# Performance work log

Measured on AMD Instinct MI355X. Metric: run time of the kernel, lower is better.

The kernel has to match this reference:

```python
import jax, jax.numpy as jnp
import numpy as np

B, S, HID = 1, 2048, 2048
H, KV, D = 32, 8, 64          # num_heads, num_kv_heads, head_dim
N_REP = H // KV               # GQA groups = 4
FF = 8192
EPS = 1e-5
ROPE_THETA = 10000.0


def _rope_tables(seq_len, dim, dtype=jnp.float32):
    inv_freq = 1.0 / (ROPE_THETA ** (jnp.arange(0, dim, 2, dtype=jnp.float32) / dim))
    t = jnp.arange(seq_len, dtype=jnp.float32)
    freqs = jnp.outer(t, inv_freq)                 # [S, D/2]
    emb = jnp.concatenate([freqs, freqs], axis=-1) # [S, D]
    return jnp.cos(emb).astype(dtype)[None], jnp.sin(emb).astype(dtype)[None]  # [1,S,D]


def setup_inputs() -> dict:
    key = jax.random.key(0)
    ks = jax.random.split(key, 10)
    s = 0.02
    cos, sin = _rope_tables(S, D)
    return {
        "hidden_states": jax.random.normal(ks[0], (B, S, HID), jnp.float32),
        "cos": cos, "sin": sin,
        "wq": jax.random.normal(ks[1], (HID, H * D), jnp.float32) * s,
        "wk": jax.random.normal(ks[2], (HID, KV * D), jnp.float32) * s,
        "wv": jax.random.normal(ks[3], (HID, KV * D), jnp.float32) * s,
        "wo": jax.random.normal(ks[4], (H * D, HID), jnp.float32) * s,
        "w_ln1": jnp.ones((HID,), jnp.float32),
        "w_ln2": jnp.ones((HID,), jnp.float32),
        "w_gate": jax.random.normal(ks[5], (HID, FF), jnp.float32) * s,
        "w_up": jax.random.normal(ks[6], (HID, FF), jnp.float32) * s,
        "w_down": jax.random.normal(ks[7], (FF, HID), jnp.float32) * s,
    }


def _rmsnorm(x, w):
    var = jnp.mean(jnp.square(x), axis=-1, keepdims=True)
    return x * jax.lax.rsqrt(var + EPS) * w


def _rotate_half(x):
    x1, x2 = jnp.split(x, 2, axis=-1)
    return jnp.concatenate([-x2, x1], axis=-1)


def _apply_rope(q, k, cos, sin):
    # q,k: [B,H,S,D]; cos,sin: [B,S,D] -> unsqueeze head dim
    c, s = cos[:, None], sin[:, None]
    return q * c + _rotate_half(q) * s, k * c + _rotate_half(k) * s


def reference(hidden_states, cos, sin, wq, wk, wv, wo, w_ln1, w_ln2, w_gate, w_up, w_down):
    residual = hidden_states
    x = _rmsnorm(hidden_states, w_ln1)

    q = (x @ wq).reshape(B, S, H, D).transpose(0, 2, 1, 3)    # [B,H,S,D]
    k = (x @ wk).reshape(B, S, KV, D).transpose(0, 2, 1, 3)   # [B,KV,S,D]
    v = (x @ wv).reshape(B, S, KV, D).transpose(0, 2, 1, 3)
    q, k = _apply_rope(q, k, cos, sin)

    # repeat_kv (interleaved) for GQA
    k = jnp.repeat(k, N_REP, axis=1)                           # [B,H,S,D]
    v = jnp.repeat(v, N_REP, axis=1)

    scale = 1.0 / np.sqrt(D)
    scores = jnp.einsum("bhqd,bhkd->bhqk", q, k) * scale       # [B,H,S,S]
    causal = jnp.tril(jnp.ones((S, S), bool))
    scores = jnp.where(causal, scores, jnp.finfo(scores.dtype).min)
    probs = jax.nn.softmax(scores, axis=-1)
    attn = jnp.einsum("bhqk,bhkd->bhqd", probs, v)             # [B,H,S,D]
    attn = attn.transpose(0, 2, 1, 3).reshape(B, S, H * D)
    attn = attn @ wo

    h = residual + attn
    residual = h
    y = _rmsnorm(h, w_ln2)
    mlp = (jax.nn.silu(y @ w_gate) * (y @ w_up)) @ w_down
    return residual + mlp
```

## Files before the change

kernel.cpp:

```cpp
#include <hip/hip_runtime.h>
#include <hip/hip_bf16.h>
#include <cstdint>

#define S_LEN 2048
#define HIDN  2048
#define NH    32
#define NKV   8
#define HD    64
#define FFN   8192
#define QKVN  3072
#define QKVLD 3072

typedef __attribute__((ext_vector_type(4)))  float f32x4;
typedef __attribute__((ext_vector_type(16))) float f32x16;
typedef __attribute__((ext_vector_type(8)))  short short8;
typedef __attribute__((ext_vector_type(4)))  short s16x4;

__device__ __forceinline__ short f2bf(float f) {
  union { float f; uint32_t u; } v; v.f = f;
  uint32_t r = v.u + 0x7FFFu + ((v.u >> 16) & 1u);
  return (short)(r >> 16);
}
__device__ __forceinline__ float bf2f(short s) {
  union { float f; uint32_t u; } v; v.u = ((uint32_t)(uint16_t)s) << 16;
  return v.f;
}
__device__ __forceinline__ unsigned packbf2(float lo, float hi) {
  return (unsigned)(uint16_t)f2bf(lo) | ((unsigned)(uint16_t)f2bf(hi) << 16);
}

#define GLOAD_LDS16(gp, lp) \
  __builtin_amdgcn_global_load_lds((const __attribute__((address_space(1))) void*)(gp), \
                                   (__attribute__((address_space(3))) void*)(lp), 16, 0, 0)

#define BARRIER()  asm volatile("s_barrier" ::: "memory")
#define LGKM0()    asm volatile("s_waitcnt lgkmcnt(0)" ::: "memory")
#define SCHED0()   __builtin_amdgcn_sched_barrier(0)
#define VMCNT(N)   asm volatile("s_waitcnt vmcnt(%0)" :: "n"(N) : "memory")

__global__ __launch_bounds__(256) void convT_kernel(const float* __restrict__ src,
    short* __restrict__ dst, int K, int N) {
  __shared__ float t[64][65];
  const int k0 = blockIdx.x * 64, n0 = blockIdx.y * 64;
  const int tr = threadIdx.x >> 4, tc = (threadIdx.x & 15) * 4;
  #pragma unroll
  for (int i = 0; i < 4; ++i) {
    float4 v = *(const float4*)(src + (size_t)(k0 + tr + i * 16) * N + n0 + tc);
    t[tr + i * 16][tc] = v.x; t[tr + i * 16][tc + 1] = v.y;
    t[tr + i * 16][tc + 2] = v.z; t[tr + i * 16][tc + 3] = v.w;
  }
  __syncthreads();
  const int dr = threadIdx.x >> 2, dc = (threadIdx.x & 3) * 16;
  short8 o0, o1;
  #pragma unroll
  for (int j = 0; j < 8; ++j) { o0[j] = f2bf(t[dc + j][dr]); o1[j] = f2bf(t[dc + 8 + j][dr]); }
  short* dp = dst + (size_t)(n0 + dr) * K + k0 + dc;
  *(short8*)dp = o0;
  *(short8*)(dp + 8) = o1;
}

__global__ __launch_bounds__(256) void convT_pack2_kernel(const float* __restrict__ wg,
    const float* __restrict__ wu, short* __restrict__ dst) {
  __shared__ float t[64][65];
  const int plane = blockIdx.z;
  const float* src = plane ? wu : wg;
  const int k0 = blockIdx.x * 64, n0 = blockIdx.y * 64;
  const int tr = threadIdx.x >> 4, tc = (threadIdx.x & 15) * 4;
  #pragma unroll
  for (int i = 0; i < 4; ++i) {
    float4 v = *(const float4*)(src + (size_t)(k0 + tr + i * 16) * FFN + n0 + tc);
    t[tr + i * 16][tc] = v.x; t[tr + i * 16][tc + 1] = v.y;
    t[tr + i * 16][tc + 2] = v.z; t[tr + i * 16][tc + 3] = v.w;
  }
  __syncthreads();
  const int dr = threadIdx.x >> 2, dc = (threadIdx.x & 3) * 16;
  const int n = n0 + dr;
  const int rr = ((n >> 4) << 5) + plane * 16 + (n & 15);
  short8 o0, o1;
  #pragma unroll
  for (int j = 0; j < 8; ++j) { o0[j] = f2bf(t[dc + j][dr]); o1[j] = f2bf(t[dc + 8 + j][dr]); }
  short* dp = dst + (size_t)rr * HIDN + k0 + dc;
  *(short8*)dp = o0;
  *(short8*)(dp + 8) = o1;
}

__global__ __launch_bounds__(256) void rmsnorm_kernel(const float* __restrict__ X,
    const float* __restrict__ W, short* __restrict__ Y) {
  int row = blockIdx.x;
  const float4* x4 = (const float4*)(X + (size_t)row * HIDN);
  const float4* w4 = (const float4*)W;
  float4 v0 = x4[2 * threadIdx.x];
  float4 v1 = x4[2 * threadIdx.x + 1];
  float ss = v0.x*v0.x + v0.y*v0.y + v0.z*v0.z + v0.w*v0.w
           + v1.x*v1.x + v1.y*v1.y + v1.z*v1.z + v1.w*v1.w;
  #pragma unroll
  for (int off = 32; off > 0; off >>= 1) ss += __shfl_xor(ss, off, 64);
  __shared__ float red[4];
  if ((threadIdx.x & 63) == 0) red[threadIdx.x >> 6] = ss;
  __syncthreads();
  ss = red[0] + red[1] + red[2] + red[3];
  float rs = rsqrtf(ss * (1.0f / HIDN) + 1e-5f);
  float4 w0 = w4[2 * threadIdx.x], w1 = w4[2 * threadIdx.x + 1];
  short8 o;
  o[0] = f2bf(v0.x * rs * w0.x); o[1] = f2bf(v0.y * rs * w0.y);
  o[2] = f2bf(v0.z * rs * w0.z); o[3] = f2bf(v0.w * rs * w0.w);
  o[4] = f2bf(v1.x * rs * w1.x); o[5] = f2bf(v1.y * rs * w1.y);
  o[6] = f2bf(v1.z * rs * w1.z); o[7] = f2bf(v1.w * rs * w1.w);
  *(short8*)(Y + (size_t)row * HIDN + threadIdx.x * 8) = o;
}

__global__ __launch_bounds__(256) void wo_norm_kernel(float* __restrict__ out,
    const float* __restrict__ hs, const short* __restrict__ P,
    const float* __restrict__ W, short* __restrict__ Y) {
  const size_t n = (size_t)S_LEN * HIDN;
  const int row = blockIdx.x;
  const size_t base = (size_t)row * HIDN + threadIdx.x * 8;
  float4 h0 = *(const float4*)(hs + base);
  float4 h1 = *(const float4*)(hs + base + 4);
  short8 a = *(const short8*)(P + base);
  short8 b = *(const short8*)(P + n + base);
  float v[8];
  v[0] = h0.x + bf2f(a[0]) + bf2f(b[0]);
  v[1] = h0.y + bf2f(a[1]) + bf2f(b[1]);
  v[2] = h0.z + bf2f(a[2]) + bf2f(b[2]);
  v[3] = h0.w + bf2f(a[3]) + bf2f(b[3]);
  v[4] = h1.x + bf2f(a[4]) + bf2f(b[4]);
  v[5] = h1.y + bf2f(a[5]) + bf2f(b[5]);
  v[6] = h1.z + bf2f(a[6]) + bf2f(b[6]);
  v[7] = h1.w + bf2f(a[7]) + bf2f(b[7]);
  float4 o0 = {v[0], v[1], v[2], v[3]}, o1 = {v[4], v[5], v[6], v[7]};
  *(float4*)(out + base) = o0;
  *(float4*)(out + base + 4) = o1;
  float ss = 0.f;
  #pragma unroll
  for (int j = 0; j < 8; ++j) ss += v[j] * v[j];
  #pragma unroll
  for (int off = 32; off > 0; off >>= 1) ss += __shfl_xor(ss, off, 64);
  __shared__ float red[4];
  if ((threadIdx.x & 63) == 0) red[threadIdx.x >> 6] = ss;
  __syncthreads();
  ss = red[0] + red[1] + red[2] + red[3];
  float rs = rsqrtf(ss * (1.0f / HIDN) + 1e-5f);
  float4 w0 = *(const float4*)(W + threadIdx.x * 8);
  float4 w1 = *(const float4*)(W + threadIdx.x * 8 + 4);
  short8 o;
  o[0] = f2bf(v[0] * rs * w0.x); o[1] = f2bf(v[1] * rs * w0.y);
  o[2] = f2bf(v[2] * rs * w0.z); o[3] = f2bf(v[3] * rs * w0.w);
  o[4] = f2bf(v[4] * rs * w1.x); o[5] = f2bf(v[5] * rs * w1.y);
  o[6] = f2bf(v[6] * rs * w1.z); o[7] = f2bf(v[7] * rs * w1.w);
  *(short8*)(Y + base) = o;
}

template<int EPI, int BN>
__global__ __launch_bounds__(512, 1) void gemm8p(const short* __restrict__ A,
    const short* __restrict__ BT, void* __restrict__ Cp, const void* __restrict__ Xp,
    int N, int Kfull, int KC, int gy) {
  constexpr int NFN = BN / 64;
  constexpr int LB  = BN / 128;
  constexpr int VN  = 2 + 2 * LB;
  __shared__ __align__(16) short As[2][256 * 64];
  __shared__ __align__(16) short Bs[2][BN * 64];
  const int tid = threadIdx.x, lane = tid & 63, w = tid >> 6;
  const int wm2 = w >> 2;
  const int wn = (w & 3) * (BN / 4);
  const int l15 = lane & 15, lg = lane >> 4;
  const int cpx = gy >> 3;
  const int xcd = blockIdx.x & 7, cid = blockIdx.x >> 3;
  const int by = xcd * cpx + cid % cpx, bx = cid / cpx;
  const int brow = bx * 256, bcol = by * BN;
  const size_t kbase = (size_t)blockIdx.z * KC;
  const int r8 = lane >> 3, c8 = lane & 7;
  const int gblk = c8 ^ r8;
  const int nt = KC / 64;
  f32x4 acc[8][NFN] = {};
  short8 af[4], bf[2][NFN];

  auto STA = [&](int p, int kt, int h) {
    const size_t kc = kbase + (size_t)kt * 64 + gblk * 8;
    #pragma unroll
    for (int j = 0; j < 2; ++j) {
      const short* g = A + (size_t)(brow + h * 128 + j * 64 + w * 8 + r8) * Kfull + kc;
      GLOAD_LDS16(g, &As[p][(h * 128 + j * 64 + w * 8) * 64]);
    }
  };
  auto STB = [&](int p, int kt, int h) {
    const size_t kc = kbase + (size_t)kt * 64 + gblk * 8;
    #pragma unroll
    for (int j = 0; j < LB; ++j) {
      const short* g = BT + (size_t)(bcol + h * (BN / 2) + j * 64 + w * 8 + r8) * Kfull + kc;
      GLOAD_LDS16(g, &Bs[p][(h * (BN / 2) + j * 64 + w * 8) * 64]);
    }
  };
  auto LDA = [&](int p, int mh, int kk) {
    #pragma unroll
    for (int m = 0; m < 4; ++m) {
      const int row = mh * 128 + wm2 * 64 + m * 16 + l15;
      af[m] = *(const short8*)&As[p][row * 64 + (((kk * 4 + lg) ^ (row & 7)) * 8)];
    }
  };
  auto LDB = [&](int p, int kk) {
    #pragma unroll
    for (int n = 0; n < NFN; ++n) {
      const int row = wn + n * 16 + l15;
      bf[kk][n] = *(const short8*)&Bs[p][row * 64 + (((kk * 4 + lg) ^ (row & 7)) * 8)];
    }
  };

#define MMQ(MH, KK) \
  __builtin_amdgcn_s_setprio(1); \
  _Pragma("unroll") \
  for (int m = 0; m < 4; ++m) \
    _Pragma("unroll") \
    for (int n = 0; n < NFN; ++n) \
      acc[(MH) * 4 + m][n] = __builtin_amdgcn_mfma_f32_16x16x32_bf16(af[m], bf[KK][n], acc[(MH) * 4 + m][n], 0, 0, 0); \
  __builtin_amdgcn_s_setprio(0);

  STB(0, 0, 0); STB(0, 0, 1); STA(0, 0, 0); STA(0, 0, 1);
  STB(1, 1, 0); STB(1, 1, 1); STA(1, 1, 0);
  VMCNT(VN);
  BARRIER();

  for (int i = 0; i < nt / 2; ++i) {
    const int t = 2 * i;
    const bool li = (i == nt / 2 - 1);
    LDA(0, 0, 0); LDB(0, 0); LDB(0, 1);
    STA(1, t + 1, 1);
    BARRIER(); LGKM0(); SCHED0();
    MMQ(0, 0);
    BARRIER();
    LDA(0, 0, 1);
    if (!li) STB(0, t + 2, 0);
    BARRIER(); LGKM0(); SCHED0();
    MMQ(0, 1);
    BARRIER();
    LDA(0, 1, 0);
    if (!li) STB(0, t + 2, 1);
    BARRIER(); LGKM0(); SCHED0();
    MMQ(1, 0);
    BARRIER();
    LDA(0, 1, 1);
    if (!li) STA(0, t + 2, 0);
    BARRIER(); LGKM0(); SCHED0();
    MMQ(1, 1);
    if (li) { VMCNT(0); } else { VMCNT(VN); }
    BARRIER();
    LDA(1, 0, 0); LDB(1, 0); LDB(1, 1);
    if (!li) STA(0, t + 2, 1);
    BARRIER(); LGKM0(); SCHED0();
    MMQ(0, 0);
    BARRIER();
    LDA(1, 0, 1);
    if (!li) STB(1, t + 3, 0);
    BARRIER(); LGKM0(); SCHED0();
    MMQ(0, 1);
    BARRIER();
    LDA(1, 1, 0);
    if (!li) STB(1, t + 3, 1);
    BARRIER(); LGKM0(); SCHED0();
    MMQ(1, 0);
    BARRIER();
    LDA(1, 1, 1);
    if (!li) STA(1, t + 3, 0);
    BARRIER(); LGKM0(); SCHED0();
    MMQ(1, 1);
    if (!li) { VMCNT(VN); }
    BARRIER();
  }
#undef MMQ

  if (EPI == 4) {
    const int No = N >> 1;
    #pragma unroll
    for (int mf = 0; mf < 8; ++mf) {
      const int r0 = brow + (mf >> 2) * 128 + wm2 * 64 + (mf & 3) * 16 + lg * 4;
      #pragma unroll
      for (int jg = 0; jg < NFN / 2; ++jg) {
        const int c = (bcol >> 1) + (wn >> 1) + jg * 16 + l15;
        #pragma unroll
        for (int i4 = 0; i4 < 4; ++i4) {
          float gt = acc[mf][2 * jg][i4];
          float up = acc[mf][2 * jg + 1][i4];
          ((short*)Cp)[(size_t)(r0 + i4) * No + c] = f2bf(gt / (1.f + __expf(-gt)) * up);
        }
      }
    }
  } else {
    #pragma unroll
    for (int mf = 0; mf < 8; ++mf) {
      const int r0 = brow + (mf >> 2) * 128 + wm2 * 64 + (mf & 3) * 16 + lg * 4;
      #pragma unroll
      for (int nf = 0; nf < NFN; ++nf) {
        const int c = bcol + wn + nf * 16 + l15;
        #pragma unroll
        for (int i4 = 0; i4 < 4; ++i4) {
          const size_t idx = (size_t)(r0 + i4) * N + c;
          float v = acc[mf][nf][i4];
          if (EPI == 0) ((short*)Cp)[idx] = f2bf(v);
          if (EPI == 1) ((float*)Cp)[idx] = v + ((const float*)Xp)[idx];
          if (EPI == 5) ((short*)Cp)[(size_t)blockIdx.z * S_LEN * N + idx] = f2bf(v);
        }
      }
    }
  }
}

__global__ __launch_bounds__(256) void rope_k_kernel(short* __restrict__ qkv,
    const float* __restrict__ cosb, const float* __restrict__ sinb) {
  int idx = blockIdx.x * 256 + threadIdx.x;
  int d = idx & 31;
  int hh = (idx >> 5) & (NKV - 1);
  int s = idx >> 8;
  short* base = qkv + (size_t)s * QKVLD + HIDN + hh * HD;
  float c  = cosb[s * HD + d];
  float sn = sinb[s * HD + d];
  float x1 = bf2f(base[d]), x2 = bf2f(base[d + 32]);
  base[d]      = f2bf(x1 * c - x2 * sn);
  base[d + 32] = f2bf(x2 * c + x1 * sn);
}

__global__ __launch_bounds__(256) void attn_kernel(const short* __restrict__ QKV,
    const float* __restrict__ cosb, const float* __restrict__ sinb,
    short* __restrict__ O) {
  __shared__ __align__(16) short Ks[128][72];
  __shared__ __align__(16) short VTs[64][136];
  const int bid = blockIdx.x;
  const int half_ = bid >> 8, idx = bid & 255;
  const int h = idx & 31;
  int qt = idx >> 5;
  qt = half_ ? (15 - qt) : qt;
  const int kvh = h >> 2;
  const int tid = threadIdx.x, lane = tid & 63, w = tid >> 6;
  const int l31 = lane & 31, hi = lane >> 5;
  const int qb = qt * 128 + w * 32;
  const int kcol = HIDN + kvh * HD;
  const int vcol = HIDN + NKV * HD + kvh * HD;

  short8 Qr[4];
  {
    const int s = qb + l31;
    const short* qp = QKV + (size_t)s * QKVLD + h * HD;
    short8 qv[4];
    #pragma unroll
    for (int dk = 0; dk < 4; ++dk) qv[dk] = *(const short8*)(qp + dk * 16 + hi * 8);
    const float* cp = cosb + s * HD;
    const float* sp = sinb + s * HD;
    #pragma unroll
    for (int dk = 0; dk < 2; ++dk)
      #pragma unroll
      for (int e = 0; e < 8; ++e) {
        const int d = dk * 16 + hi * 8 + e;
        float c = cp[d], sn = sp[d];
        float x1 = bf2f(qv[dk][e]), x2 = bf2f(qv[dk + 2][e]);
        Qr[dk][e]     = f2bf((x1 * c - x2 * sn) * 0.125f);
        Qr[dk + 2][e] = f2bf((x2 * c + x1 * sn) * 0.125f);
      }
  }
  float m_ = -3e38f, l_ = 0.f;
  f32x16 o0 = {}, o1 = {};
  const int nt = qt + 1;
  const int kr_ = tid >> 1, kdb = (tid & 1) * 32;

  short8 kr0, kr1, kr2, kr3, vr0, vr1, vr2, vr3;
  {
    const short* gk = QKV + (size_t)kr_ * QKVLD + kcol + kdb;
    kr0 = *(const short8*)gk;        kr1 = *(const short8*)(gk + 8);
    kr2 = *(const short8*)(gk + 16); kr3 = *(const short8*)(gk + 24);
    const short* gv = QKV + (size_t)kr_ * QKVLD + vcol + kdb;
    vr0 = *(const short8*)gv;        vr1 = *(const short8*)(gv + 8);
    vr2 = *(const short8*)(gv + 16); vr3 = *(const short8*)(gv + 24);
  }

  for (int t = 0; t < nt; ++t) {
    const int kb = t * 128;
    BARRIER();
    {
      short8* kp = (short8*)&Ks[kr_][kdb];
      kp[0] = kr0; kp[1] = kr1; kp[2] = kr2; kp[3] = kr3;
      #pragma unroll
      for (int j = 0; j < 8; ++j) VTs[kdb + j][kr_]      = vr0[j];
      #pragma unroll
      for (int j = 0; j < 8; ++j) VTs[kdb + 8 + j][kr_]  = vr1[j];
      #pragma unroll
      for (int j = 0; j < 8; ++j) VTs[kdb + 16 + j][kr_] = vr2[j];
      #pragma unroll
      for (int j = 0; j < 8; ++j) VTs[kdb + 24 + j][kr_] = vr3[j];
    }
    LGKM0();
    BARRIER();
    if (t + 1 < nt) {
      const int kb2 = kb + 128;
      const short* gk = QKV + (size_t)(kb2 + kr_) * QKVLD + kcol + kdb;
      kr0 = *(const short8*)gk;        kr1 = *(const short8*)(gk + 8);
      kr2 = *(const short8*)(gk + 16); kr3 = *(const short8*)(gk + 24);
      const short* gv = QKV + (size_t)(kb2 + kr_) * QKVLD + vcol + kdb;
      vr0 = *(const short8*)gv;        vr1 = *(const short8*)(gv + 8);
      vr2 = *(const short8*)(gv + 16); vr3 = *(const short8*)(gv + 24);
    }
    #pragma unroll
    for (int hf = 0; hf < 2; ++hf) {
      const int hb = kb + hf * 64;
      if (hb < qb + 32) {
        f32x16 s[2] = {};
        __builtin_amdgcn_s_setprio(1);
        #pragma unroll
        for (int kt = 0; kt < 2; ++kt)
          #pragma unroll
          for (int dk = 0; dk < 4; ++dk) {
            short8 kf = *(const short8*)&Ks[hf * 64 + kt * 32 + l31][dk * 16 + hi * 8];
            s[kt] = __builtin_amdgcn_mfma_f32_32x32x16_bf16(kf, Qr[dk], s[kt], 0, 0, 0);
          }
        __builtin_amdgcn_s_setprio(0);
        if (hb + 63 > qb) {
          const int qg = qb + l31;
          #pragma unroll
          for (int kt = 0; kt < 2; ++kt)
            #pragma unroll
            for (int r = 0; r < 16; ++r) {
              const int kg = hb + kt * 32 + (r & 3) + 8 * (r >> 2) + 4 * hi;
              if (kg > qg) s[kt][r] = -1e30f;
            }
        }
        float pm = s[0][0];
        #pragma unroll
        for (int r = 1; r < 16; ++r) pm = fmaxf(pm, s[0][r]);
        #pragma unroll
        for (int r = 0; r < 16; ++r) pm = fmaxf(pm, s[1][r]);
        pm = fmaxf(pm, __shfl_xor(pm, 32));
        const float mn = fmaxf(m_, pm);
        const float al = __expf(m_ - mn);
        float rsum = 0.f;
        #pragma unroll
        for (int kt = 0; kt < 2; ++kt)
          #pragma unroll
          for (int r = 0; r < 16; ++r) { s[kt][r] = __expf(s[kt][r] - mn); rsum += s[kt][r]; }
        rsum += __shfl_xor(rsum, 32);
        l_ = l_ * al + rsum;
        m_ = mn;
        o0 *= al; o1 *= al;
        unsigned wd[2][8], rw[2][8];
        #pragma unroll
        for (int kt = 0; kt < 2; ++kt)
          #pragma unroll
          for (int i = 0; i < 8; ++i) {
            wd[kt][i] = packbf2(s[kt][2 * i], s[kt][2 * i + 1]);
            rw[kt][i] = (unsigned)__shfl_xor((int)wd[kt][i], 32);
          }
        #pragma unroll
        for (int kt = 0; kt < 2; ++kt) {
          union { unsigned u[4]; short8 s8; } pf0, pf1;
          if (hi) {
            pf0.u[0] = rw[kt][2]; pf0.u[1] = rw[kt][3]; pf0.u[2] = wd[kt][2]; pf0.u[3] = wd[kt][3];
            pf1.u[0] = rw[kt][6]; pf1.u[1] = rw[kt][7]; pf1.u[2] = wd[kt][6]; pf1.u[3] = wd[kt][7];
          } else {
            pf0.u[0] = wd[kt][0]; pf0.u[1] = wd[kt][1]; pf0.u[2] = rw[kt][0]; pf0.u[3] = rw[kt][1];
            pf1.u[0] = wd[kt][4]; pf1.u[1] = wd[kt][5]; pf1.u[2] = rw[kt][4]; pf1.u[3] = rw[kt][5];
          }
          __builtin_amdgcn_s_setprio(1);
          #pragma unroll
          for (int ks = 0; ks < 2; ++ks) {
            const short8 pB = ks ? pf1.s8 : pf0.s8;
            short8 va = *(const short8*)&VTs[l31][hf * 64 + kt * 32 + ks * 16 + hi * 8];
            o0 = __builtin_amdgcn_mfma_f32_32x32x16_bf16(va, pB, o0, 0, 0, 0);
            short8 vb = *(const short8*)&VTs[32 + l31][hf * 64 + kt * 32 + ks * 16 + hi * 8];
            o1 = __builtin_amdgcn_mfma_f32_32x32x16_bf16(vb, pB, o1, 0, 0, 0);
          }
          __builtin_amdgcn_s_setprio(0);
        }
      }
    }
  }
  const float inv = 1.f / l_;
  short* op = O + (size_t)(qb + l31) * HIDN + h * HD;
  #pragma unroll
  for (int dt = 0; dt < 2; ++dt) {
    const f32x16& o = dt ? o1 : o0;
    #pragma unroll
    for (int g = 0; g < 4; ++g) {
      s16x4 st;
      st[0] = f2bf(o[g * 4 + 0] * inv);
      st[1] = f2bf(o[g * 4 + 1] * inv);
      st[2] = f2bf(o[g * 4 + 2] * inv);
      st[3] = f2bf(o[g * 4 + 3] * inv);
      *(s16x4*)(op + dt * 32 + g * 8 + hi * 4) = st;
    }
  }
}

__global__ __launch_bounds__(256) void reduce4_kernel(float* __restrict__ out,
    const short* __restrict__ P) {
  const size_t n = (size_t)S_LEN * HIDN;
  size_t i = ((size_t)blockIdx.x * 256 + threadIdx.x) * 4;
  float4 o = *(float4*)(out + i);
  float s0 = 0.f, s1 = 0.f, s2 = 0.f, s3 = 0.f;
  #pragma unroll
  for (int z = 0; z < 4; ++z) {
    s16x4 p = *(const s16x4*)(P + z * n + i);
    s0 += bf2f(p[0]); s1 += bf2f(p[1]); s2 += bf2f(p[2]); s3 += bf2f(p[3]);
  }
  o.x += s0; o.y += s1; o.z += s2; o.w += s3;
  *(float4*)(out + i) = o;
}

extern "C" void kernel_launch(void* const* d_in, const int* in_sizes, int n_in,
                              void* d_out, int out_size, void* d_ws, size_t ws_size,
                              hipStream_t stream) {
  const float* hs   = (const float*)d_in[0];
  const float* cosb = (const float*)d_in[1];
  const float* sinb = (const float*)d_in[2];
  const float* wq   = (const float*)d_in[3];
  const float* wk   = (const float*)d_in[4];
  const float* wv   = (const float*)d_in[5];
  const float* wo   = (const float*)d_in[6];
  const float* wln1 = (const float*)d_in[7];
  const float* wln2 = (const float*)d_in[8];
  const float* wg   = (const float*)d_in[9];
  const float* wu   = (const float*)d_in[10];
  const float* wd   = (const float*)d_in[11];
  float* out = (float*)d_out;
  char* ws = (char*)d_ws;
  const size_t MB = 1024 * 1024;
  short* Wbig  = (short*)(ws);
  short* Wqkv  = Wbig;
  short* xn    = (short*)(ws + 13 * MB);
  short* qkv   = (short*)(ws + 21 * MB);
  short* attnO = (short*)(ws + 34 * MB);
  short* Wwo   = (short*)(ws + 42 * MB);
  short* Pwo   = (short*)(ws);
  short* y     = (short*)(ws + 64 * MB);
  short* g     = (short*)(ws + 72 * MB);
  short* Wd    = Wbig;
  short* P     = (short*)(ws + 32 * MB);

  convT_kernel<<<dim3(32, 32), 256, 0, stream>>>(wq, Wqkv, HIDN, NH * HD);
  convT_kernel<<<dim3(32, 8),  256, 0, stream>>>(wk, Wqkv + (size_t)2048 * HIDN, HIDN, NKV * HD);
  convT_kernel<<<dim3(32, 8),  256, 0, stream>>>(wv, Wqkv + (size_t)2560 * HIDN, HIDN, NKV * HD);
  rmsnorm_kernel<<<S_LEN, 256, 0, stream>>>(hs, wln1, xn);
  gemm8p<0, 128><<<dim3(192, 1, 1), 512, 0, stream>>>(xn, Wqkv, qkv, nullptr, QKVN, HIDN, HIDN, 24);
  convT_kernel<<<dim3(32, 32), 256, 0, stream>>>(wo, Wwo, NH * HD, HIDN);
  rope_k_kernel<<<(S_LEN * NKV * 32) / 256, 256, 0, stream>>>(qkv, cosb, sinb);
  attn_kernel<<<NH * (S_LEN / 128), 256, 0, stream>>>(qkv, cosb, sinb, attnO);
  gemm8p<5, 128><<<dim3(128, 1, 2), 512, 0, stream>>>(attnO, Wwo, Pwo, nullptr, HIDN, NH * HD, NH * HD / 2, 16);
  wo_norm_kernel<<<S_LEN, 256, 0, stream>>>(out, hs, Pwo, wln2, y);
  convT_pack2_kernel<<<dim3(32, 128, 2), 256, 0, stream>>>(wg, wu, Wbig);
  gemm8p<4, 256><<<dim3(512, 1, 1), 512, 0, stream>>>(y, Wbig, g, nullptr, 2 * FFN, HIDN, HIDN, 64);
  convT_kernel<<<dim3(128, 32), 256, 0, stream>>>(wd, Wd, FFN, HIDN);
  gemm8p<5, 256><<<dim3(64, 1, 4), 512, 0, stream>>>(g, Wd, P, nullptr, HIDN, FFN, FFN / 4, 8);
  reduce4_kernel<<<(S_LEN * HIDN) / 1024, 256, 0, stream>>>(out, P);
}
```

Measured before the change: 408.7 us.

## Swizzle attention K/V LDS layout and split-K the QKV projection GEMM

```diff
diff --git a/kernel.cpp b/kernel.cpp
--- a/kernel.cpp
+++ b/kernel.cpp
@@ -27,6 +27,9 @@
 }
 __device__ __forceinline__ unsigned packbf2(float lo, float hi) {
   return (unsigned)(uint16_t)f2bf(lo) | ((unsigned)(uint16_t)f2bf(hi) << 16);
+}
+__device__ __forceinline__ unsigned packs2(short lo, short hi) {
+  return (unsigned)(uint16_t)lo | ((unsigned)(uint16_t)hi << 16);
 }
 
 #define GLOAD_LDS16(gp, lp) \
@@ -304,6 +307,18 @@
   }
 }
 
+__global__ __launch_bounds__(256) void reduce_qkv_kernel(short* __restrict__ qkv,
+    const short* __restrict__ P) {
+  const size_t n = (size_t)S_LEN * QKVN;
+  size_t i = ((size_t)blockIdx.x * 256 + threadIdx.x) * 8;
+  short8 a = *(const short8*)(P + i);
+  short8 b = *(const short8*)(P + n + i);
+  short8 o;
+  #pragma unroll
+  for (int j = 0; j < 8; ++j) o[j] = f2bf(bf2f(a[j]) + bf2f(b[j]));
+  *(short8*)(qkv + i) = o;
+}
+
 __global__ __launch_bounds__(256) void rope_k_kernel(short* __restrict__ qkv,
     const float* __restrict__ cosb, const float* __restrict__ sinb) {
   int idx = blockIdx.x * 256 + threadIdx.x;
@@ -321,8 +336,8 @@
 __global__ __launch_bounds__(256) void attn_kernel(const short* __restrict__ QKV,
     const float* __restrict__ cosb, const float* __restrict__ sinb,
     short* __restrict__ O) {
-  __shared__ __align__(16) short Ks[128][72];
-  __shared__ __align__(16) short VTs[64][136];
+  __shared__ __align__(16) short Ks[128 * 64];
+  __shared__ __align__(16) short VTs[64 * 128];
   const int bid = blockIdx.x;
   const int half_ = bid >> 8, idx = bid & 255;
   const int h = idx & 31;
@@ -358,43 +373,50 @@
   float m_ = -3e38f, l_ = 0.f;
   f32x16 o0 = {}, o1 = {};
   const int nt = qt + 1;
-  const int kr_ = tid >> 1, kdb = (tid & 1) * 32;
-
-  short8 kr0, kr1, kr2, kr3, vr0, vr1, vr2, vr3;
+  const int kr_ = tid >> 1, kdb1 = (tid & 1);
+  const int va_ = tid & 63, vdb = (tid >> 6) * 16;
+
+  short8 kp0, kp1, kp2, kp3, vp0, vp1, vp2, vp3;
   {
-    const short* gk = QKV + (size_t)kr_ * QKVLD + kcol + kdb;
-    kr0 = *(const short8*)gk;        kr1 = *(const short8*)(gk + 8);
-    kr2 = *(const short8*)(gk + 16); kr3 = *(const short8*)(gk + 24);
-    const short* gv = QKV + (size_t)kr_ * QKVLD + vcol + kdb;
-    vr0 = *(const short8*)gv;        vr1 = *(const short8*)(gv + 8);
-    vr2 = *(const short8*)(gv + 16); vr3 = *(const short8*)(gv + 24);
+    const short* gk = QKV + (size_t)kr_ * QKVLD + kcol + kdb1 * 32;
+    kp0 = *(const short8*)gk;        kp1 = *(const short8*)(gk + 8);
+    kp2 = *(const short8*)(gk + 16); kp3 = *(const short8*)(gk + 24);
+    const short* gv0 = QKV + (size_t)(2 * va_) * QKVLD + vcol + vdb;
+    const short* gv1 = QKV + (size_t)(2 * va_ + 1) * QKVLD + vcol + vdb;
+    vp0 = *(const short8*)gv0; vp1 = *(const short8*)(gv0 + 8);
+    vp2 = *(const short8*)gv1; vp3 = *(const short8*)(gv1 + 8);
   }
 
   for (int t = 0; t < nt; ++t) {
     const int kb = t * 128;
     BARRIER();
     {
-      short8* kp = (short8*)&Ks[kr_][kdb];
-      kp[0] = kr0; kp[1] = kr1; kp[2] = kr2; kp[3] = kr3;
+      short* kbase_ = Ks + kr_ * 64;
+      const int rs = kr_ & 7;
+      *(short8*)(kbase_ + ((kdb1 * 4 + 0) ^ rs) * 8) = kp0;
+      *(short8*)(kbase_ + ((kdb1 * 4 + 1) ^ rs) * 8) = kp1;
+      *(short8*)(kbase_ + ((kdb1 * 4 + 2) ^ rs) * 8) = kp2;
+      *(short8*)(kbase_ + ((kdb1 * 4 + 3) ^ rs) * 8) = kp3;
+      const int kblk = (2 * va_) >> 3, kin = (2 * va_) & 7;
       #pragma unroll
-      for (int j = 0; j < 8; ++j) VTs[kdb + j][kr_]      = vr0[j];
-      #pragma unroll
-      for (int j = 0; j < 8; ++j) VTs[kdb + 8 + j][kr_]  = vr1[j];
-      #pragma unroll
-      for (int j = 0; j < 8; ++j) VTs[kdb + 16 + j][kr_] = vr2[j];
-      #pragma unroll
-      for (int j = 0; j < 8; ++j) VTs[kdb + 24 + j][kr_] = vr3[j];
+      for (int j = 0; j < 8; ++j) {
+        const int d0 = vdb + j;
+        *(unsigned*)(VTs + d0 * 128 + ((kblk ^ (d0 & 7)) * 8) + kin) = packs2(vp0[j], vp2[j]);
+        const int d1 = vdb + 8 + j;
+        *(unsigned*)(VTs + d1 * 128 + ((kblk ^ (d1 & 7)) * 8) + kin) = packs2(vp1[j], vp3[j]);
+      }
     }
     LGKM0();
     BARRIER();
     if (t + 1 < nt) {
       const int kb2 = kb + 128;
-      const short* gk = QKV + (size_t)(kb2 + kr_) * QKVLD + kcol + kdb;
-      kr0 = *(const short8*)gk;        kr1 = *(const short8*)(gk + 8);
-      kr2 = *(const short8*)(gk + 16); kr3 = *(const short8*)(gk + 24);
-      const short* gv = QKV + (size_t)(kb2 + kr_) * QKVLD + vcol + kdb;
-      vr0 = *(const short8*)gv;        vr1 = *(const short8*)(gv + 8);
-      vr2 = *(const short8*)(gv + 16); vr3 = *(const short8*)(gv + 24);
+      const short* gk = QKV + (size_t)(kb2 + kr_) * QKVLD + kcol + kdb1 * 32;
+      kp0 = *(const short8*)gk;        kp1 = *(const short8*)(gk + 8);
+      kp2 = *(const short8*)(gk + 16); kp3 = *(const short8*)(gk + 24);
+      const short* gv0 = QKV + (size_t)(kb2 + 2 * va_) * QKVLD + vcol + vdb;
+      const short* gv1 = QKV + (size_t)(kb2 + 2 * va_ + 1) * QKVLD + vcol + vdb;
+      vp0 = *(const short8*)gv0; vp1 = *(const short8*)(gv0 + 8);
+      vp2 = *(const short8*)gv1; vp3 = *(const short8*)(gv1 + 8);
     }
     #pragma unroll
     for (int hf = 0; hf < 2; ++hf) {
@@ -403,12 +425,14 @@
         f32x16 s[2] = {};
         __builtin_amdgcn_s_setprio(1);
         #pragma unroll
-        for (int kt = 0; kt < 2; ++kt)
+        for (int kt = 0; kt < 2; ++kt) {
+          const int row = hf * 64 + kt * 32 + l31;
           #pragma unroll
           for (int dk = 0; dk < 4; ++dk) {
-            short8 kf = *(const short8*)&Ks[hf * 64 + kt * 32 + l31][dk * 16 + hi * 8];
+            short8 kf = *(const short8*)(Ks + row * 64 + (((dk * 2 + hi) ^ (row & 7)) * 8));
             s[kt] = __builtin_amdgcn_mfma_f32_32x32x16_bf16(kf, Qr[dk], s[kt], 0, 0, 0);
           }
+        }
         __builtin_amdgcn_s_setprio(0);
         if (hb + 63 > qb) {
           const int qg = qb + l31;
@@ -459,9 +483,11 @@
           #pragma unroll
           for (int ks = 0; ks < 2; ++ks) {
             const short8 pB = ks ? pf1.s8 : pf0.s8;
-            short8 va = *(const short8*)&VTs[l31][hf * 64 + kt * 32 + ks * 16 + hi * 8];
+            const int blk = hf * 8 + kt * 4 + ks * 2 + hi;
+            const int d0 = l31, d1 = 32 + l31;
+            short8 va = *(const short8*)(VTs + d0 * 128 + ((blk ^ (d0 & 7)) * 8));
             o0 = __builtin_amdgcn_mfma_f32_32x32x16_bf16(va, pB, o0, 0, 0, 0);
-            short8 vb = *(const short8*)&VTs[32 + l31][hf * 64 + kt * 32 + ks * 16 + hi * 8];
+            short8 vb = *(const short8*)(VTs + d1 * 128 + ((blk ^ (d1 & 7)) * 8));
             o1 = __builtin_amdgcn_mfma_f32_32x32x16_bf16(vb, pB, o1, 0, 0, 0);
           }
           __builtin_amdgcn_s_setprio(0);
@@ -519,23 +545,25 @@
   float* out = (float*)d_out;
   char* ws = (char*)d_ws;
   const size_t MB = 1024 * 1024;
-  short* Wbig  = (short*)(ws);
-  short* Wqkv  = Wbig;
+  short* Wqkv  = (short*)(ws);
   short* xn    = (short*)(ws + 13 * MB);
   short* qkv   = (short*)(ws + 21 * MB);
   short* attnO = (short*)(ws + 34 * MB);
-  short* Wwo   = (short*)(ws + 42 * MB);
-  short* Pwo   = (short*)(ws);
+  short* Pqkv  = (short*)(ws + 36 * MB);
+  short* Wwo   = (short*)(ws);
+  short* Pwo   = (short*)(ws + 8 * MB);
   short* y     = (short*)(ws + 64 * MB);
   short* g     = (short*)(ws + 72 * MB);
-  short* Wd    = Wbig;
+  short* Wbig  = (short*)(ws);
+  short* Wd    = (short*)(ws);
   short* P     = (short*)(ws + 32 * MB);
 
   convT_kernel<<<dim3(32, 32), 256, 0, stream>>>(wq, Wqkv, HIDN, NH * HD);
   convT_kernel<<<dim3(32, 8),  256, 0, stream>>>(wk, Wqkv + (size_t)2048 * HIDN, HIDN, NKV * HD);
   convT_kernel<<<dim3(32, 8),  256, 0, stream>>>(wv, Wqkv + (size_t)2560 * HIDN, HIDN, NKV * HD);
   rmsnorm_kernel<<<S_LEN, 256, 0, stream>>>(hs, wln1, xn);
-  gemm8p<0, 128><<<dim3(192, 1, 1), 512, 0, stream>>>(xn, Wqkv, qkv, nullptr, QKVN, HIDN, HIDN, 24);
+  gemm8p<5, 128><<<dim3(192, 1, 2), 512, 0, stream>>>(xn, Wqkv, Pqkv, nullptr, QKVN, HIDN, HIDN / 2, 24);
+  reduce_qkv_kernel<<<(S_LEN * QKVN) / 2048, 256, 0, stream>>>(qkv, Pqkv);
   convT_kernel<<<dim3(32, 32), 256, 0, stream>>>(wo, Wwo, NH * HD, HIDN);
   rope_k_kernel<<<(S_LEN * NKV * 32) / 256, 256, 0, stream>>>(qkv, cosb, sinb);
   attn_kernel<<<NH * (S_LEN / 128), 256, 0, stream>>>(qkv, cosb, sinb, attnO);
```

Measured after the change: 418.6 us. +2.4%, slower.
